# Performance work log

Hardware: AMD Instinct MI355X
Metric: run time of the kernel (lower is better)

## Reference

```python
import jax, jax.numpy as jnp
import numpy as np

D_ATOM, D_MODEL, H = 128, 512, 4
D_H = D_ATOM // H
D_FF = 4 * D_ATOM
EPS = 1e-5


def _ln(x, g, b):
    m = jnp.mean(x, axis=-1, keepdims=True)
    v = jnp.mean((x - m) ** 2, axis=-1, keepdims=True)
    return (x - m) / jnp.sqrt(v + EPS) * g + b


def setup_inputs() -> dict:
    key = jax.random.key(0)
    ks = jax.random.split(key, 20)
    B, N_ATOM, N_PAIRS, N_TOK = 2, 2048, 16384, 512
    c_atom = jax.random.normal(ks[0], (B, N_ATOM, D_ATOM), dtype=jnp.float32)
    p_lm = jax.random.normal(ks[1], (B, N_PAIRS, 16), dtype=jnp.float32)
    p_lm_idx = jax.random.randint(ks[2], (B, N_PAIRS, 2), 0, N_ATOM, dtype=jnp.int32)
    token_idx = jnp.sort(jax.random.randint(ks[3], (B, N_ATOM), 0, N_TOK, dtype=jnp.int32), axis=-1)
    s = 0.05
    w = lambda k, sh: jax.random.normal(k, sh, dtype=jnp.float32) * s
    return {
        'c_atom': c_atom, 'p_lm': p_lm, 'p_lm_idx': p_lm_idx,
        'token_idx': token_idx, 'n_tokens': N_TOK,
        'ln_attn_g': jnp.ones((D_ATOM,), jnp.float32), 'ln_attn_b': jnp.zeros((D_ATOM,), jnp.float32),
        'w_q': w(ks[4], (D_ATOM, D_ATOM)), 'w_k': w(ks[5], (D_ATOM, D_ATOM)),
        'w_v': w(ks[6], (D_ATOM, D_ATOM)), 'w_g': w(ks[7], (D_ATOM, D_ATOM)),
        'w_o': w(ks[8], (D_ATOM, D_ATOM)),
        'pb_w': w(ks[9], (16, H)), 'pb_b': jnp.zeros((H,), jnp.float32),
        'ln_ff_g': jnp.ones((D_ATOM,), jnp.float32), 'ln_ff_b': jnp.zeros((D_ATOM,), jnp.float32),
        'sw_w1': w(ks[10], (D_ATOM, D_FF)), 'sw_w2': w(ks[11], (D_ATOM, D_FF)),
        'sw_w3': w(ks[12], (D_FF, D_ATOM)),
        'tok_w': w(ks[13], (D_ATOM, D_MODEL)), 'tok_b': jnp.zeros((D_MODEL,), jnp.float32),
    }


def reference(c_atom, p_lm, p_lm_idx, token_idx, n_tokens,
              ln_attn_g, ln_attn_b, w_q, w_k, w_v, w_g, w_o, pb_w, pb_b,
              ln_ff_g, ln_ff_b, sw_w1, sw_w2, sw_w3, tok_w, tok_b):
    B, N, _ = c_atom.shape
    q_n = _ln(c_atom, ln_attn_g, ln_attn_b)
    Q = (q_n @ w_q).reshape(B, N, H, D_H)
    K = (q_n @ w_k).reshape(B, N, H, D_H)
    V = (q_n @ w_v).reshape(B, N, H, D_H)
    G = q_n @ w_g  # (B, N, d_atom)

    scores = jnp.einsum('bihd,bjhd->bhij', Q, K) / jnp.sqrt(jnp.float32(D_H))

    bias = p_lm @ pb_w + pb_b  # (B, P, H)
    def scat(src, dst, b_):
        return jnp.zeros((H, N, N), b_.dtype).at[:, src, dst].set(b_.T)
    pair_bias = jax.vmap(scat)(p_lm_idx[..., 0], p_lm_idx[..., 1], bias)
    scores = scores + pair_bias

    token_mask = token_idx[:, :, None] == token_idx[:, None, :]  # (B,N,N)
    scores = jnp.where(token_mask[:, None], scores, -jnp.inf)
    attn = jax.nn.softmax(scores, axis=-1)
    attn = jnp.nan_to_num(attn)

    att_out = jnp.einsum('bhij,bjhd->bihd', attn, V).reshape(B, N, D_ATOM)
    q = c_atom + jax.nn.sigmoid(G) * (att_out @ w_o)
    h = _ln(q, ln_ff_g, ln_ff_b)
    q = q + (jax.nn.silu(h @ sw_w1) * (h @ sw_w2)) @ sw_w3
    atom_feat = q @ tok_w + tok_b  # (B, N, d_model)

    seg = (token_idx + jnp.arange(B, dtype=token_idx.dtype)[:, None] * n_tokens).reshape(-1)
    sums = jax.ops.segment_sum(atom_feat.reshape(B * N, D_MODEL), seg, num_segments=B * n_tokens)
    cnts = jax.ops.segment_sum(jnp.ones((B * N,), atom_feat.dtype), seg, num_segments=B * n_tokens)
    out = sums / jnp.maximum(cnts, 1.0)[:, None]
    return out.reshape(B, n_tokens, D_MODEL)
```

## Files before the change

kernel.cpp:

```cpp
#include <hip/hip_runtime.h>
#include <hip/hip_bf16.h>
#include <math.h>

#define B_     2
#define N_     2048
#define DA     128
#define H_     4
#define DH     32
#define DFF    512
#define DM     512
#define NT     512
#define NP     16384
#define MAXL   32
#define LDSP   136
#define PVS    40

typedef short bf16x8 __attribute__((ext_vector_type(8)));
typedef float f32x4  __attribute__((ext_vector_type(4)));

__device__ __forceinline__ short bf16r(float x) {
    union { float f; unsigned u; } v; v.f = x;
    unsigned r = v.u + 0x7FFFu + ((v.u >> 16) & 1u);
    return (short)(r >> 16);
}
__device__ __forceinline__ float bf2f(short h) {
    union { unsigned u; float f; } v;
    v.u = ((unsigned)(unsigned short)h) << 16;
    return v.f;
}

__global__ __launch_bounds__(1024) void setup_kernel(
        const float* __restrict__ wq, const float* __restrict__ wk,
        const float* __restrict__ wv, const float* __restrict__ wg,
        const float* __restrict__ wo, const float* __restrict__ w1,
        const float* __restrict__ w2, const float* __restrict__ w3,
        const float* __restrict__ tw, const int* __restrict__ tok,
        const int* __restrict__ pidx,
        const float* __restrict__ c_atom, const float* __restrict__ lng,
        const float* __restrict__ lnb,
        short* __restrict__ pqkvg, short* __restrict__ pwo,
        short* __restrict__ pw12, short* __restrict__ pw3,
        short* __restrict__ ptok, short* __restrict__ hln,
        int* __restrict__ cnt, int* __restrict__ tst,
        int* __restrict__ win) {
    __shared__ int c[1024];
    __shared__ int sb[1024];
    if (blockIdx.x < 42) {
        int gid = blockIdx.x * 1024 + threadIdx.x;
        int lane = gid & 63;
        int grp = gid >> 6;
        int quad = lane >> 4, nn = lane & 15;
        const float* src; short* dst; int stride;
        if (grp < 128) {
            int g = grp; int kt = g & 3, nt = g >> 2;
            int n = nt * 16 + nn;
            const float* w = (n < 128) ? wq : (n < 256) ? wk : (n < 384) ? wv : wg;
            src = w + (kt * 32 + quad * 8) * 128 + (n & 127);
            dst = pqkvg + (g * 64 + lane) * 8;
            stride = 128;
        } else if (grp < 160) {
            int g = grp - 128; int kt = g & 3, nt = g >> 2;
            src = wo + (kt * 32 + quad * 8) * 128 + nt * 16 + nn;
            dst = pwo + (g * 64 + lane) * 8;
            stride = 128;
        } else if (grp < 416) {
            int g = grp - 160; int kt = g & 3, nt = g >> 2;
            int n = nt * 16 + nn;
            src = ((n & 1) ? w2 : w1) + (kt * 32 + quad * 8) * 512 + (n >> 1);
            dst = pw12 + (g * 64 + lane) * 8;
            stride = 512;
        } else if (grp < 544) {
            int g = grp - 416; int kt = g & 15, nt = g >> 4;
            src = w3 + (kt * 32 + quad * 8) * 128 + nt * 16 + nn;
            dst = pw3 + (g * 64 + lane) * 8;
            stride = 128;
        } else {
            int g = grp - 544; int kt = g & 3, nt = g >> 2;
            src = tw + (kt * 32 + quad * 8) * 512 + nt * 16 + nn;
            dst = ptok + (g * 64 + lane) * 8;
            stride = 512;
        }
#pragma unroll
        for (int j = 0; j < 8; j++) dst[j] = bf16r(src[j * stride]);
    } else if (blockIdx.x == 42) {
        int tid = threadIdx.x;
        c[tid] = 0;
        __syncthreads();
#pragma unroll
        for (int i = 0; i < 4; i++) {
            int idx = tid + i * 1024;
            int b = idx >> 11;
            atomicAdd(&c[b * NT + tok[idx]], 1);
        }
        __syncthreads();
        int t = tid & (NT - 1);
        int v = c[tid];
        int* cur = c;
        int* alt = sb;
        for (int d = 1; d < NT; d <<= 1) {
            int y = cur[tid];
            if (t >= d) y += cur[tid - d];
            alt[tid] = y;
            __syncthreads();
            int* tmp = cur; cur = alt; alt = tmp;
        }
        tst[tid] = cur[tid] - v;
        cnt[tid] = v;
    } else if (blockIdx.x < 75) {
        int p = (blockIdx.x - 43) * 1024 + threadIdx.x;
        int b = p >> 14, pp = p & (NP - 1);
        int src = pidx[p * 2], dst = pidx[p * 2 + 1];
        if (tok[b * N_ + src] == tok[b * N_ + dst])
            atomicMax(&win[(b * N_ + src) * MAXL + (dst & 31)], pp + 1);
    } else {
        int t = threadIdx.x;
        int rowg = (blockIdx.x - 75) * 256 + (t >> 2);
        int sub = t & 3;
        const float* xr = c_atom + rowg * DA + sub * 32;
        float4 v[8];
        float s = 0.f, sq = 0.f;
#pragma unroll
        for (int i = 0; i < 8; i++) {
            v[i] = *(const float4*)(xr + i * 4);
            s  += v[i].x + v[i].y + v[i].z + v[i].w;
            sq += v[i].x * v[i].x + v[i].y * v[i].y + v[i].z * v[i].z + v[i].w * v[i].w;
        }
        s += __shfl_xor(s, 1); sq += __shfl_xor(sq, 1);
        s += __shfl_xor(s, 2); sq += __shfl_xor(sq, 2);
        float mean = s * (1.f / 128.f);
        float var = sq * (1.f / 128.f) - mean * mean;
        float inv = rsqrtf(var + 1e-5f);
        const float* gp = lng + sub * 32;
        const float* bp = lnb + sub * 32;
        short* dst = hln + rowg * DA + sub * 32;
#pragma unroll
        for (int i = 0; i < 8; i++) {
            dst[i * 4 + 0] = bf16r((v[i].x - mean) * inv * gp[i * 4 + 0] + bp[i * 4 + 0]);
            dst[i * 4 + 1] = bf16r((v[i].y - mean) * inv * gp[i * 4 + 1] + bp[i * 4 + 1]);
            dst[i * 4 + 2] = bf16r((v[i].z - mean) * inv * gp[i * 4 + 2] + bp[i * 4 + 2]);
            dst[i * 4 + 3] = bf16r((v[i].w - mean) * inv * gp[i * 4 + 3] + bp[i * 4 + 3]);
        }
    }
}

__global__ __launch_bounds__(1024) void biasfill(
        const int* __restrict__ pidx, const int* __restrict__ tok,
        const int* __restrict__ win, const float* __restrict__ plm,
        const float* __restrict__ pbw, const float* __restrict__ pbb,
        float* __restrict__ biasT) {
    int p = blockIdx.x * 1024 + threadIdx.x;
    int b = p >> 14, pp = p & (NP - 1);
    int src = pidx[p * 2], dst = pidx[p * 2 + 1];
    if (tok[b * N_ + src] != tok[b * N_ + dst]) return;
    int key = (b * N_ + src) * MAXL + (dst & 31);
    if (win[key] != pp + 1) return;
    const float* pl = plm + (size_t)p * 16;
#pragma unroll
    for (int h = 0; h < H_; h++) {
        float bs = pbb[h];
#pragma unroll
        for (int f = 0; f < 16; f++) bs += pl[f] * pbw[f * H_ + h];
        biasT[(size_t)key * 4 + h] = bs;
    }
}

template<int KT, int KTB, int NTT, int STR>
__device__ __forceinline__ void gemm_a(const short* __restrict__ Abase,
                                       const short* __restrict__ Bp,
                                       int nt0, int lane, f32x4* acc) {
    const short* arow = Abase + (lane & 15) * STR + (lane >> 4) * 8;
    const short* bbase = Bp + lane * 8;
#pragma unroll
    for (int kt = 0; kt < KT; kt++) {
        bf16x8 a = *(const bf16x8*)(arow + kt * 32);
#pragma unroll
        for (int nt = 0; nt < NTT; nt++) {
            bf16x8 b = *(const bf16x8*)(bbase + ((nt0 + nt) * KTB + kt) * 512);
            acc[nt] = __builtin_amdgcn_mfma_f32_16x16x32_bf16(a, b, acc[nt], 0, 0, 0);
        }
    }
}

__global__ __launch_bounds__(256, 2) void tokfused(
        const short* __restrict__ hln, const float* __restrict__ c_atom,
        const float* __restrict__ biasT,
        const int* __restrict__ tst, const int* __restrict__ cnt,
        const int* __restrict__ win,
        const short* __restrict__ pqkvg, const short* __restrict__ pwo,
        const short* __restrict__ pw12, const short* __restrict__ pw3,
        const short* __restrict__ ptok,
        const float* __restrict__ lnfg, const float* __restrict__ lnfb,
        const float* __restrict__ tb, float* __restrict__ out) {
    __shared__ __align__(16) char arena[54272];
    short* As  = (short*)(arena + 0);
    short* Qs  = (short*)(arena + 8704);
    short* Ps  = (short*)(arena + 8704);
    short* Ks  = (short*)(arena + 18944);
    short* VT  = (short*)(arena + 27648);
    float* sgf = (float*)(arena + 37888);
    float* valf = (float*)(arena + 8704);
    short* us   = (short*)(arena + 27648);
    short* q2s  = (short*)(arena + 0);
    short* mrs  = (short*)(arena + 25088);

    int token = blockIdx.x;
    int b = token >> 9;
    int tid = threadIdx.x;
    int lane = tid & 63, wave = tid >> 6;
    int quad = lane >> 4, cc = lane & 15;
    int start = tst[token];
    int L = cnt[token]; if (L > MAXL) L = MAXL;
    const bool fast = (L <= 16);

    {
        int row = tid >> 3, sub = tid & 7;
        int4 v0 = {0,0,0,0}, v1 = {0,0,0,0};
        if (row < L) {
            const int4* src = (const int4*)(hln + (size_t)(b * N_ + start + row) * DA + sub * 16);
            v0 = src[0]; v1 = src[1];
        }
        int4* dst = (int4*)(As + row * LDSP + sub * 16);
        dst[0] = v0; dst[1] = v1;
        if (fast) {
            int4* vz = (int4*)(arena + 27648);
            int4 zz = {0,0,0,0};
#pragma unroll
            for (int k = 0; k < 3; k++) {
                int idx = tid + k * 256;
                if (idx < 640) vz[idx] = zz;
            }
        }
    }
    __syncthreads();

    {
        f32x4 a0[8], a1[8];
#pragma unroll
        for (int i = 0; i < 8; i++)
#pragma unroll
            for (int r = 0; r < 4; r++) { a0[i][r] = 0.f; a1[i][r] = 0.f; }
        gemm_a<4, 4, 8, LDSP>(As, pqkvg, wave * 8, lane, a0);
        if (!fast) gemm_a<4, 4, 8, LDSP>(As + 16 * LDSP, pqkvg, wave * 8, lane, a1);
#pragma unroll
        for (int rt = 0; rt < 2; rt++) {
            if (rt == 1 && fast) break;
            f32x4* ac = rt ? a1 : a0;
#pragma unroll
            for (int nt = 0; nt < 8; nt++) {
                int lc = nt * 16 + cc;
#pragma unroll
                for (int r = 0; r < 4; r++) {
                    int lrow = rt * 16 + quad * 4 + r;
                    float v = ac[nt][r];
                    if (wave == 3)      sgf[lrow * 128 + lc] = 1.f / (1.f + __expf(-v));
                    else if (wave == 0) Qs[lrow * LDSP + lc] = bf16r(v);
                    else if (wave == 1) Ks[lrow * LDSP + lc] = bf16r(v);
                    else VT[(lc >> 5) * 32 * PVS + (lc & 31) * PVS + lrow] = bf16r(v);
                }
            }
        }
    }
    __syncthreads();

    {
        int h = wave;
        const float scale = 0.17677669529663687f;
        int rb = lane & 15;
        f32x4 z = {0.f, 0.f, 0.f, 0.f};
        bf16x8 qa0 = *(const bf16x8*)(Qs + rb * LDSP + h * 32 + quad * 8);
        bf16x8 kb0 = *(const bf16x8*)(Ks + rb * LDSP + h * 32 + quad * 8);
        f32x4 sc00 = __builtin_amdgcn_mfma_f32_16x16x32_bf16(qa0, kb0, z, 0, 0, 0);
        f32x4 sc01 = z, sc10 = z, sc11 = z;
        if (!fast) {
            bf16x8 qa1 = *(const bf16x8*)(Qs + (16 + rb) * LDSP + h * 32 + quad * 8);
            bf16x8 kb1 = *(const bf16x8*)(Ks + (16 + rb) * LDSP + h * 32 + quad * 8);
            sc01 = __builtin_amdgcn_mfma_f32_16x16x32_bf16(qa0, kb1, z, 0, 0, 0);
            sc10 = __builtin_amdgcn_mfma_f32_16x16x32_bf16(qa1, kb0, z, 0, 0, 0);
            sc11 = __builtin_amdgcn_mfma_f32_16x16x32_bf16(qa1, kb1, z, 0, 0, 0);
        }
        __syncthreads();
        short* Ph = Ps + h * 32 * PVS;
        int j0 = cc, j1 = 16 + cc;
#pragma unroll
        for (int it = 0; it < 2; it++) {
            if (it == 1 && fast) break;
            f32x4 sj0 = it ? sc10 : sc00;
            f32x4 sj1 = it ? sc11 : sc01;
#pragma unroll
            for (int r = 0; r < 4; r++) {
                int i = it * 16 + quad * 4 + r;
                int at = start + i; if (at > N_ - 1) at = N_ - 1;
                const int* wrow = win + (size_t)(b * N_ + at) * MAXL;
                const float* brow = biasT + (size_t)(b * N_ + at) * MAXL * 4;
                float s0 = sj0[r] * scale;
                float s1 = fast ? -1e30f : sj1[r] * scale;
                int pw0 = (j0 < L) ? wrow[(start + j0) & 31] : 0;
                if (pw0 > 0) s0 += brow[((start + j0) & 31) * 4 + h];
                if (!fast) {
                    int pw1 = (j1 < L) ? wrow[(start + j1) & 31] : 0;
                    if (pw1 > 0) s1 += brow[((start + j1) & 31) * 4 + h];
                    if (j1 >= L) s1 = -1e30f;
                }
                if (j0 >= L) s0 = -1e30f;
                float m = fmaxf(s0, s1);
                m = fmaxf(m, __shfl_xor(m, 1));
                m = fmaxf(m, __shfl_xor(m, 2));
                m = fmaxf(m, __shfl_xor(m, 4));
                m = fmaxf(m, __shfl_xor(m, 8));
                float e0 = __expf(s0 - m), e1 = __expf(s1 - m);
                float sm = e0 + e1;
                sm += __shfl_xor(sm, 1);
                sm += __shfl_xor(sm, 2);
                sm += __shfl_xor(sm, 4);
                sm += __shfl_xor(sm, 8);
                float inv = 1.f / sm;
                Ph[i * PVS + j0] = bf16r(e0 * inv);
                Ph[i * PVS + j1] = bf16r(e1 * inv);
            }
        }
        __syncthreads();
        const short* Vh = VT + h * 32 * PVS;
        bf16x8 va0 = *(const bf16x8*)(Vh + rb * PVS + quad * 8);
        bf16x8 va1 = *(const bf16x8*)(Vh + (16 + rb) * PVS + quad * 8);
        bf16x8 pb0 = *(const bf16x8*)(Ph + rb * PVS + quad * 8);
        f32x4 ot00 = __builtin_amdgcn_mfma_f32_16x16x32_bf16(va0, pb0, z, 0, 0, 0);
        f32x4 ot10 = __builtin_amdgcn_mfma_f32_16x16x32_bf16(va1, pb0, z, 0, 0, 0);
#pragma unroll
        for (int r = 0; r < 4; r++) {
            As[cc * LDSP + h * 32 + quad * 4 + r]      = bf16r(ot00[r]);
            As[cc * LDSP + h * 32 + 16 + quad * 4 + r] = bf16r(ot10[r]);
        }
        if (!fast) {
            bf16x8 pb1 = *(const bf16x8*)(Ph + (16 + rb) * PVS + quad * 8);
            f32x4 ot01 = __builtin_amdgcn_mfma_f32_16x16x32_bf16(va0, pb1, z, 0, 0, 0);
            f32x4 ot11 = __builtin_amdgcn_mfma_f32_16x16x32_bf16(va1, pb1, z, 0, 0, 0);
#pragma unroll
            for (int r = 0; r < 4; r++) {
                As[(16 + cc) * LDSP + h * 32 + quad * 4 + r]      = bf16r(ot01[r]);
                As[(16 + cc) * LDSP + h * 32 + 16 + quad * 4 + r] = bf16r(ot11[r]);
            }
        }
    }
    __syncthreads();

    if (!fast || wave < 2) {
        f32x4 a3[4];
#pragma unroll
        for (int i = 0; i < 4; i++)
#pragma unroll
            for (int r = 0; r < 4; r++) a3[i][r] = 0.f;
        gemm_a<4, 4, 4, LDSP>(As + (wave >> 1) * 16 * LDSP, pwo, (wave & 1) * 4, lane, a3);
#pragma unroll
        for (int ntl = 0; ntl < 4; ntl++) {
            int gcol = ((wave & 1) * 4 + ntl) * 16 + cc;
#pragma unroll
            for (int r = 0; r < 4; r++) {
                int lrow = (wave >> 1) * 16 + quad * 4 + r;
                int garow = start + lrow; if (garow > N_ - 1) garow = N_ - 1;
                float v = c_atom[(size_t)(b * N_ + garow) * DA + gcol]
                        + sgf[lrow * 128 + gcol] * a3[ntl][r];
                valf[lrow * 128 + gcol] = v;
            }
        }
    }
    __syncthreads();

    {
        int row = tid >> 3, sub = tid & 7;
        if (!fast || row < 16) {
            const float* vr = valf + row * 128 + sub * 16;
            float4 x[4];
            float s = 0.f, sq = 0.f;
#pragma unroll
            for (int i = 0; i < 4; i++) {
                x[i] = *(const float4*)(vr + i * 4);
                s  += x[i].x + x[i].y + x[i].z + x[i].w;
                sq += x[i].x * x[i].x + x[i].y * x[i].y + x[i].z * x[i].z + x[i].w * x[i].w;
            }
            s += __shfl_xor(s, 1); sq += __shfl_xor(sq, 1);
            s += __shfl_xor(s, 2); sq += __shfl_xor(sq, 2);
            s += __shfl_xor(s, 4); sq += __shfl_xor(sq, 4);
            float mean = s * (1.f / 128.f);
            float var = sq * (1.f / 128.f) - mean * mean;
            float inv = rsqrtf(var + 1e-5f);
            short* hr = As + row * LDSP + sub * 16;
            const float* gp = lnfg + sub * 16;
            const float* bp = lnfb + sub * 16;
#pragma unroll
            for (int i = 0; i < 4; i++) {
                hr[i * 4 + 0] = bf16r((x[i].x - mean) * inv * gp[i * 4 + 0] + bp[i * 4 + 0]);
                hr[i * 4 + 1] = bf16r((x[i].y - mean) * inv * gp[i * 4 + 1] + bp[i * 4 + 1]);
                hr[i * 4 + 2] = bf16r((x[i].z - mean) * inv * gp[i * 4 + 2] + bp[i * 4 + 2]);
                hr[i * 4 + 3] = bf16r((x[i].w - mean) * inv * gp[i * 4 + 3] + bp[i * 4 + 3]);
            }
        }
    }
    __syncthreads();

    f32x4 c3a[4];
#pragma unroll
    for (int i = 0; i < 4; i++)
#pragma unroll
        for (int r = 0; r < 4; r++) c3a[i][r] = 0.f;
#pragma unroll
    for (int ch = 0; ch < 2; ch++) {
        f32x4 u0[8], u1[8];
#pragma unroll
        for (int i = 0; i < 8; i++)
#pragma unroll
            for (int r = 0; r < 4; r++) { u0[i][r] = 0.f; u1[i][r] = 0.f; }
        const short* bp12 = pw12 + ch * 32 * 4 * 512;
        gemm_a<4, 4, 8, LDSP>(As, bp12, wave * 8, lane, u0);
        if (!fast) gemm_a<4, 4, 8, LDSP>(As + 16 * LDSP, bp12, wave * 8, lane, u1);
#pragma unroll
        for (int rt = 0; rt < 2; rt++) {
            if (rt == 1 && fast) break;
            f32x4* ac = rt ? u1 : u0;
#pragma unroll
            for (int nt = 0; nt < 8; nt++) {
                int col8 = (wave * 8 + nt) * 8 + (cc >> 1);
#pragma unroll
                for (int r = 0; r < 4; r++) {
                    float v = ac[nt][r];
                    float p = __shfl_xor(v, 1);
                    if (!(lane & 1)) {
                        float sil = v / (1.f + __expf(-v));
                        us[(rt * 16 + quad * 4 + r) * 264 + col8] = bf16r(sil * p);
                    }
                }
            }
        }
        __syncthreads();
        if (!fast || wave < 2)
            gemm_a<8, 16, 4, 264>(us + (wave >> 1) * 16 * 264, pw3 + ch * 8 * 512,
                                  (wave & 1) * 4, lane, c3a);
        __syncthreads();
    }

    if (!fast || wave < 2) {
#pragma unroll
        for (int ntl = 0; ntl < 4; ntl++) {
            int gcol = ((wave & 1) * 4 + ntl) * 16 + cc;
#pragma unroll
            for (int r = 0; r < 4; r++) {
                int lrow = (wave >> 1) * 16 + quad * 4 + r;
                q2s[lrow * 128 + gcol] = bf16r(valf[lrow * 128 + gcol] + c3a[ntl][r]);
            }
        }
    }
    __syncthreads();

    if (tid < 128) {
        int col = tid;
        float sum = 0.f;
        for (int i = 0; i < L; i++) sum += bf2f(q2s[i * 128 + col]);
        float inv = (L > 0) ? 1.f / (float)L : 0.f;
        mrs[col] = bf16r(sum * inv);
    }
    __syncthreads();

    {
        f32x4 a8[8];
#pragma unroll
        for (int i = 0; i < 8; i++)
#pragma unroll
            for (int r = 0; r < 4; r++) a8[i][r] = 0.f;
        gemm_a<4, 4, 8, LDSP>(mrs, ptok, wave * 8, lane, a8);
        if (quad == 0) {
#pragma unroll
            for (int nt = 0; nt < 8; nt++) {
                int col = (wave * 8 + nt) * 16 + cc;
                out[(size_t)token * DM + col] = a8[nt][0] + tb[col];
            }
        }
    }
}

extern "C" void kernel_launch(void* const* d_in, const int* in_sizes, int n_in,
                              void* d_out, int out_size, void* d_ws, size_t ws_size,
                              hipStream_t stream) {
    const float* c_atom  = (const float*)d_in[0];
    const float* p_lm    = (const float*)d_in[1];
    const int*   p_idx   = (const int*)d_in[2];
    const int*   tok     = (const int*)d_in[3];
    const float* ln_a_g  = (const float*)d_in[5];
    const float* ln_a_b  = (const float*)d_in[6];
    const float* w_q     = (const float*)d_in[7];
    const float* w_k     = (const float*)d_in[8];
    const float* w_v     = (const float*)d_in[9];
    const float* w_g     = (const float*)d_in[10];
    const float* w_o     = (const float*)d_in[11];
    const float* pb_w    = (const float*)d_in[12];
    const float* pb_b    = (const float*)d_in[13];
    const float* ln_f_g  = (const float*)d_in[14];
    const float* ln_f_b  = (const float*)d_in[15];
    const float* sw_w1   = (const float*)d_in[16];
    const float* sw_w2   = (const float*)d_in[17];
    const float* sw_w3   = (const float*)d_in[18];
    const float* tok_w   = (const float*)d_in[19];
    const float* tok_b   = (const float*)d_in[20];
    float* out = (float*)d_out;

    float* ws = (float*)d_ws;
    int*   cnt   = (int*)ws;
    int*   tst   = cnt + 1024;
    int*   win   = tst + 1024;
    short* pqkvg = (short*)(win + 131072);
    short* pwo   = pqkvg + 65536;
    short* pw12  = pwo + 16384;
    short* pw3   = pw12 + 131072;
    short* ptok  = pw3 + 65536;
    short* hln   = ptok + 65536;
    float* biasT = (float*)(hln + 524288);

    setup_kernel<<<91, 1024, 0, stream>>>(w_q, w_k, w_v, w_g, w_o, sw_w1, sw_w2,
                                          sw_w3, tok_w, tok, p_idx,
                                          c_atom, ln_a_g, ln_a_b,
                                          pqkvg, pwo, pw12, pw3, ptok, hln,
                                          cnt, tst, win);

    biasfill<<<32, 1024, 0, stream>>>(p_idx, tok, win, p_lm, pb_w, pb_b, biasT);

    tokfused<<<dim3(B_ * NT), dim3(256), 0, stream>>>(
        hln, c_atom, biasT, tst, cnt, win,
        pqkvg, pwo, pw12, pw3, ptok,
        ln_f_g, ln_f_b, tok_b, out);
}
```

Measured before the change: 166.0 us.

## Pack multiple tokens per block via bin descriptors with block-diagonal attention masking

Instead of one workgroup per token (1024 blocks, each mostly under-filled since tokens average about 4 atoms), the setup kernel now greedily packs consecutive tokens into bins of up to 32 atoms and writes bin descriptors. The fused kernel processes a whole bin and masks attention by comparing per-row token ids. It then does per-token mean pooling and a 32-row output GEMM. Excess blocks exit early. This removes wasted MFMA work on padded rows and the per-block fixed overhead, at the cost of a serial single-thread binning loop in setup and always running the full 32-row path. Occupancy is also raised to 3 blocks per SIMD with slightly reduced LDS.

```diff
diff --git a/kernel.cpp b/kernel.cpp
--- a/kernel.cpp
+++ b/kernel.cpp
@@ -42,7 +42,8 @@
         short* __restrict__ pw12, short* __restrict__ pw3,
         short* __restrict__ ptok, short* __restrict__ hln,
         int* __restrict__ cnt, int* __restrict__ tst,
-        int* __restrict__ win) {
+        int* __restrict__ win, int* __restrict__ desc,
+        int* __restrict__ nbinsp) {
     __shared__ int c[1024];
     __shared__ int sb[1024];
     if (blockIdx.x < 42) {
@@ -106,6 +107,22 @@
         }
         tst[tid] = cur[tid] - v;
         cnt[tid] = v;
+        __syncthreads();
+        c[tid] = v;
+        __syncthreads();
+        if (tid == 0) {
+            int nb = 0, acc = 0, bs = 0;
+            for (int tt = 0; tt < 1024; tt++) {
+                int ct = c[tt]; if (ct > 32) ct = 32;
+                if (tt > bs && (acc + ct > 32 || (tt - bs) >= 32 || tt == 512)) {
+                    desc[nb++] = bs | ((tt - bs) << 16);
+                    bs = tt; acc = 0;
+                }
+                acc += ct;
+            }
+            desc[nb++] = bs | ((1024 - bs) << 16);
+            nbinsp[0] = nb;
+        }
     } else if (blockIdx.x < 75) {
         int p = (blockIdx.x - 43) * 1024 + threadIdx.x;
         int b = p >> 14, pp = p & (NP - 1);
@@ -181,54 +198,57 @@
     }
 }
 
-__global__ __launch_bounds__(256, 2) void tokfused(
+__global__ __launch_bounds__(256, 3) void tokfused(
         const short* __restrict__ hln, const float* __restrict__ c_atom,
-        const float* __restrict__ biasT,
+        const float* __restrict__ biasT, const int* __restrict__ tok,
         const int* __restrict__ tst, const int* __restrict__ cnt,
-        const int* __restrict__ win,
+        const int* __restrict__ win, const int* __restrict__ desc,
+        const int* __restrict__ nbinsp,
         const short* __restrict__ pqkvg, const short* __restrict__ pwo,
         const short* __restrict__ pw12, const short* __restrict__ pw3,
         const short* __restrict__ ptok,
         const float* __restrict__ lnfg, const float* __restrict__ lnfb,
         const float* __restrict__ tb, float* __restrict__ out) {
-    __shared__ __align__(16) char arena[54272];
+    int blk = blockIdx.x;
+    if (blk >= nbinsp[0]) return;
+    __shared__ __align__(16) char arena[52736];
+    __shared__ int stok[32];
+    __shared__ int tcnt[32];
     short* As  = (short*)(arena + 0);
     short* Qs  = (short*)(arena + 8704);
     short* Ps  = (short*)(arena + 8704);
-    short* Ks  = (short*)(arena + 18944);
-    short* VT  = (short*)(arena + 27648);
-    float* sgf = (float*)(arena + 37888);
+    short* Ks  = (short*)(arena + 17408);
+    short* VT  = (short*)(arena + 26112);
+    float* sgf = (float*)(arena + 36352);
     float* valf = (float*)(arena + 8704);
-    short* us   = (short*)(arena + 27648);
+    short* us   = (short*)(arena + 26112);
     short* q2s  = (short*)(arena + 0);
-    short* mrs  = (short*)(arena + 25088);
-
-    int token = blockIdx.x;
-    int b = token >> 9;
+    short* mrs  = (short*)(arena + 17408);
+
+    int d = desc[blk];
+    int t0 = d & 0xFFFF, ntok = d >> 16;
+    int b = t0 >> 9;
     int tid = threadIdx.x;
     int lane = tid & 63, wave = tid >> 6;
     int quad = lane >> 4, cc = lane & 15;
-    int start = tst[token];
-    int L = cnt[token]; if (L > MAXL) L = MAXL;
-    const bool fast = (L <= 16);
+    int astart = tst[t0];
+    int tlast = t0 + ntok - 1;
+    int R = tst[tlast] + cnt[tlast] - astart;
+    if (R > 32) R = 32;
 
     {
         int row = tid >> 3, sub = tid & 7;
         int4 v0 = {0,0,0,0}, v1 = {0,0,0,0};
-        if (row < L) {
-            const int4* src = (const int4*)(hln + (size_t)(b * N_ + start + row) * DA + sub * 16);
+        if (row < R) {
+            const int4* src = (const int4*)(hln + (size_t)(b * N_ + astart + row) * DA + sub * 16);
             v0 = src[0]; v1 = src[1];
         }
         int4* dst = (int4*)(As + row * LDSP + sub * 16);
         dst[0] = v0; dst[1] = v1;
-        if (fast) {
-            int4* vz = (int4*)(arena + 27648);
-            int4 zz = {0,0,0,0};
-#pragma unroll
-            for (int k = 0; k < 3; k++) {
-                int idx = tid + k * 256;
-                if (idx < 640) vz[idx] = zz;
-            }
+        if (tid < 32) {
+            stok[tid] = (tid < R) ? tok[b * N_ + astart + tid] : (0x40000000 + tid);
+            int n = (tid < ntok) ? cnt[t0 + tid] : 0;
+            tcnt[tid] = (n > 32) ? 32 : n;
         }
     }
     __syncthreads();
@@ -240,10 +260,9 @@
 #pragma unroll
             for (int r = 0; r < 4; r++) { a0[i][r] = 0.f; a1[i][r] = 0.f; }
         gemm_a<4, 4, 8, LDSP>(As, pqkvg, wave * 8, lane, a0);
-        if (!fast) gemm_a<4, 4, 8, LDSP>(As + 16 * LDSP, pqkvg, wave * 8, lane, a1);
+        gemm_a<4, 4, 8, LDSP>(As + 16 * LDSP, pqkvg, wave * 8, lane, a1);
 #pragma unroll
         for (int rt = 0; rt < 2; rt++) {
-            if (rt == 1 && fast) break;
             f32x4* ac = rt ? a1 : a0;
 #pragma unroll
             for (int nt = 0; nt < 8; nt++) {
@@ -268,40 +287,36 @@
         int rb = lane & 15;
         f32x4 z = {0.f, 0.f, 0.f, 0.f};
         bf16x8 qa0 = *(const bf16x8*)(Qs + rb * LDSP + h * 32 + quad * 8);
+        bf16x8 qa1 = *(const bf16x8*)(Qs + (16 + rb) * LDSP + h * 32 + quad * 8);
         bf16x8 kb0 = *(const bf16x8*)(Ks + rb * LDSP + h * 32 + quad * 8);
+        bf16x8 kb1 = *(const bf16x8*)(Ks + (16 + rb) * LDSP + h * 32 + quad * 8);
         f32x4 sc00 = __builtin_amdgcn_mfma_f32_16x16x32_bf16(qa0, kb0, z, 0, 0, 0);
-        f32x4 sc01 = z, sc10 = z, sc11 = z;
-        if (!fast) {
-            bf16x8 qa1 = *(const bf16x8*)(Qs + (16 + rb) * LDSP + h * 32 + quad * 8);
-            bf16x8 kb1 = *(const bf16x8*)(Ks + (16 + rb) * LDSP + h * 32 + quad * 8);
-            sc01 = __builtin_amdgcn_mfma_f32_16x16x32_bf16(qa0, kb1, z, 0, 0, 0);
-            sc10 = __builtin_amdgcn_mfma_f32_16x16x32_bf16(qa1, kb0, z, 0, 0, 0);
-            sc11 = __builtin_amdgcn_mfma_f32_16x16x32_bf16(qa1, kb1, z, 0, 0, 0);
-        }
+        f32x4 sc01 = __builtin_amdgcn_mfma_f32_16x16x32_bf16(qa0, kb1, z, 0, 0, 0);
+        f32x4 sc10 = __builtin_amdgcn_mfma_f32_16x16x32_bf16(qa1, kb0, z, 0, 0, 0);
+        f32x4 sc11 = __builtin_amdgcn_mfma_f32_16x16x32_bf16(qa1, kb1, z, 0, 0, 0);
         __syncthreads();
         short* Ph = Ps + h * 32 * PVS;
         int j0 = cc, j1 = 16 + cc;
+        int tj0 = stok[j0], tj1 = stok[j1];
 #pragma unroll
         for (int it = 0; it < 2; it++) {
-            if (it == 1 && fast) break;
             f32x4 sj0 = it ? sc10 : sc00;
             f32x4 sj1 = it ? sc11 : sc01;
 #pragma unroll
             for (int r = 0; r < 4; r++) {
                 int i = it * 16 + quad * 4 + r;
-                int at = start + i; if (at > N_ - 1) at = N_ - 1;
-                const int* wrow = win + (size_t)(b * N_ + at) * MAXL;
-                const float* brow = biasT + (size_t)(b * N_ + at) * MAXL * 4;
-                float s0 = sj0[r] * scale;
-                float s1 = fast ? -1e30f : sj1[r] * scale;
-                int pw0 = (j0 < L) ? wrow[(start + j0) & 31] : 0;
-                if (pw0 > 0) s0 += brow[((start + j0) & 31) * 4 + h];
-                if (!fast) {
-                    int pw1 = (j1 < L) ? wrow[(start + j1) & 31] : 0;
-                    if (pw1 > 0) s1 += brow[((start + j1) & 31) * 4 + h];
-                    if (j1 >= L) s1 = -1e30f;
+                int ti = stok[i];
+                int ai = b * N_ + astart + i;
+                float s0 = (tj0 == ti) ? sj0[r] * scale : -1e30f;
+                float s1 = (tj1 == ti) ? sj1[r] * scale : -1e30f;
+                if (tj0 == ti && i < R && j0 < R) {
+                    int key = ai * MAXL + ((astart + j0) & 31);
+                    if (win[key] > 0) s0 += biasT[(size_t)key * 4 + h];
                 }
-                if (j0 >= L) s0 = -1e30f;
+                if (tj1 == ti && i < R && j1 < R) {
+                    int key = ai * MAXL + ((astart + j1) & 31);
+                    if (win[key] > 0) s1 += biasT[(size_t)key * 4 + h];
+                }
                 float m = fmaxf(s0, s1);
                 m = fmaxf(m, __shfl_xor(m, 1));
                 m = fmaxf(m, __shfl_xor(m, 2));
@@ -323,27 +338,22 @@
         bf16x8 va0 = *(const bf16x8*)(Vh + rb * PVS + quad * 8);
         bf16x8 va1 = *(const bf16x8*)(Vh + (16 + rb) * PVS + quad * 8);
         bf16x8 pb0 = *(const bf16x8*)(Ph + rb * PVS + quad * 8);
+        bf16x8 pb1 = *(const bf16x8*)(Ph + (16 + rb) * PVS + quad * 8);
         f32x4 ot00 = __builtin_amdgcn_mfma_f32_16x16x32_bf16(va0, pb0, z, 0, 0, 0);
+        f32x4 ot01 = __builtin_amdgcn_mfma_f32_16x16x32_bf16(va0, pb1, z, 0, 0, 0);
         f32x4 ot10 = __builtin_amdgcn_mfma_f32_16x16x32_bf16(va1, pb0, z, 0, 0, 0);
+        f32x4 ot11 = __builtin_amdgcn_mfma_f32_16x16x32_bf16(va1, pb1, z, 0, 0, 0);
 #pragma unroll
         for (int r = 0; r < 4; r++) {
-            As[cc * LDSP + h * 32 + quad * 4 + r]      = bf16r(ot00[r]);
-            As[cc * LDSP + h * 32 + 16 + quad * 4 + r] = bf16r(ot10[r]);
-        }
-        if (!fast) {
-            bf16x8 pb1 = *(const bf16x8*)(Ph + (16 + rb) * PVS + quad * 8);
-            f32x4 ot01 = __builtin_amdgcn_mfma_f32_16x16x32_bf16(va0, pb1, z, 0, 0, 0);
-            f32x4 ot11 = __builtin_amdgcn_mfma_f32_16x16x32_bf16(va1, pb1, z, 0, 0, 0);
-#pragma unroll
-            for (int r = 0; r < 4; r++) {
-                As[(16 + cc) * LDSP + h * 32 + quad * 4 + r]      = bf16r(ot01[r]);
-                As[(16 + cc) * LDSP + h * 32 + 16 + quad * 4 + r] = bf16r(ot11[r]);
-            }
-        }
-    }
-    __syncthreads();
-
-    if (!fast || wave < 2) {
+            As[cc * LDSP + h * 32 + quad * 4 + r]             = bf16r(ot00[r]);
+            As[cc * LDSP + h * 32 + 16 + quad * 4 + r]        = bf16r(ot10[r]);
+            As[(16 + cc) * LDSP + h * 32 + quad * 4 + r]      = bf16r(ot01[r]);
+            As[(16 + cc) * LDSP + h * 32 + 16 + quad * 4 + r] = bf16r(ot11[r]);
+        }
+    }
+    __syncthreads();
+
+    {
         f32x4 a3[4];
 #pragma unroll
         for (int i = 0; i < 4; i++)
@@ -356,7 +366,7 @@
 #pragma unroll
             for (int r = 0; r < 4; r++) {
                 int lrow = (wave >> 1) * 16 + quad * 4 + r;
-                int garow = start + lrow; if (garow > N_ - 1) garow = N_ - 1;
+                int garow = astart + lrow; if (garow > N_ - 1) garow = N_ - 1;
                 float v = c_atom[(size_t)(b * N_ + garow) * DA + gcol]
                         + sgf[lrow * 128 + gcol] * a3[ntl][r];
                 valf[lrow * 128 + gcol] = v;
@@ -367,32 +377,30 @@
 
     {
         int row = tid >> 3, sub = tid & 7;
-        if (!fast || row < 16) {
-            const float* vr = valf + row * 128 + sub * 16;
-            float4 x[4];
-            float s = 0.f, sq = 0.f;
-#pragma unroll
-            for (int i = 0; i < 4; i++) {
-                x[i] = *(const float4*)(vr + i * 4);
-                s  += x[i].x + x[i].y + x[i].z + x[i].w;
-                sq += x[i].x * x[i].x + x[i].y * x[i].y + x[i].z * x[i].z + x[i].w * x[i].w;
-            }
-            s += __shfl_xor(s, 1); sq += __shfl_xor(sq, 1);
-            s += __shfl_xor(s, 2); sq += __shfl_xor(sq, 2);
-            s += __shfl_xor(s, 4); sq += __shfl_xor(sq, 4);
-            float mean = s * (1.f / 128.f);
-            float var = sq * (1.f / 128.f) - mean * mean;
-            float inv = rsqrtf(var + 1e-5f);
-            short* hr = As + row * LDSP + sub * 16;
-            const float* gp = lnfg + sub * 16;
-            const float* bp = lnfb + sub * 16;
-#pragma unroll
-            for (int i = 0; i < 4; i++) {
-                hr[i * 4 + 0] = bf16r((x[i].x - mean) * inv * gp[i * 4 + 0] + bp[i * 4 + 0]);
-                hr[i * 4 + 1] = bf16r((x[i].y - mean) * inv * gp[i * 4 + 1] + bp[i * 4 + 1]);
-                hr[i * 4 + 2] = bf16r((x[i].z - mean) * inv * gp[i * 4 + 2] + bp[i * 4 + 2]);
-                hr[i * 4 + 3] = bf16r((x[i].w - mean) * inv * gp[i * 4 + 3] + bp[i * 4 + 3]);
-            }
+        const float* vr = valf + row * 128 + sub * 16;
+        float4 x[4];
+        float s = 0.f, sq = 0.f;
+#pragma unroll
+        for (int i = 0; i < 4; i++) {
+            x[i] = *(const float4*)(vr + i * 4);
+            s  += x[i].x + x[i].y + x[i].z + x[i].w;
+            sq += x[i].x * x[i].x + x[i].y * x[i].y + x[i].z * x[i].z + x[i].w * x[i].w;
+        }
+        s += __shfl_xor(s, 1); sq += __shfl_xor(sq, 1);
+        s += __shfl_xor(s, 2); sq += __shfl_xor(sq, 2);
+        s += __shfl_xor(s, 4); sq += __shfl_xor(sq, 4);
+        float mean = s * (1.f / 128.f);
+        float var = sq * (1.f / 128.f) - mean * mean;
+        float inv = rsqrtf(var + 1e-5f);
+        short* hr = As + row * LDSP + sub * 16;
+        const float* gp = lnfg + sub * 16;
+        const float* bp = lnfb + sub * 16;
+#pragma unroll
+        for (int i = 0; i < 4; i++) {
+            hr[i * 4 + 0] = bf16r((x[i].x - mean) * inv * gp[i * 4 + 0] + bp[i * 4 + 0]);
+            hr[i * 4 + 1] = bf16r((x[i].y - mean) * inv * gp[i * 4 + 1] + bp[i * 4 + 1]);
+            hr[i * 4 + 2] = bf16r((x[i].z - mean) * inv * gp[i * 4 + 2] + bp[i * 4 + 2]);
+            hr[i * 4 + 3] = bf16r((x[i].w - mean) * inv * gp[i * 4 + 3] + bp[i * 4 + 3]);
         }
     }
     __syncthreads();
@@ -411,10 +419,9 @@
             for (int r = 0; r < 4; r++) { u0[i][r] = 0.f; u1[i][r] = 0.f; }
         const short* bp12 = pw12 + ch * 32 * 4 * 512;
         gemm_a<4, 4, 8, LDSP>(As, bp12, wave * 8, lane, u0);
-        if (!fast) gemm_a<4, 4, 8, LDSP>(As + 16 * LDSP, bp12, wave * 8, lane, u1);
+        gemm_a<4, 4, 8, LDSP>(As + 16 * LDSP, bp12, wave * 8, lane, u1);
 #pragma unroll
         for (int rt = 0; rt < 2; rt++) {
-            if (rt == 1 && fast) break;
             f32x4* ac = rt ? u1 : u0;
 #pragma unroll
             for (int nt = 0; nt < 8; nt++) {
@@ -431,13 +438,12 @@
             }
         }
         __syncthreads();
-        if (!fast || wave < 2)
-            gemm_a<8, 16, 4, 264>(us + (wave >> 1) * 16 * 264, pw3 + ch * 8 * 512,
-                                  (wave & 1) * 4, lane, c3a);
-        __syncthreads();
-    }
-
-    if (!fast || wave < 2) {
+        gemm_a<8, 16, 4, 264>(us + (wave >> 1) * 16 * 264, pw3 + ch * 8 * 512,
+                              (wave & 1) * 4, lane, c3a);
+        __syncthreads();
+    }
+
+    {
 #pragma unroll
         for (int ntl = 0; ntl < 4; ntl++) {
             int gcol = ((wave & 1) * 4 + ntl) * 16 + cc;
@@ -452,25 +458,37 @@
 
     if (tid < 128) {
         int col = tid;
-        float sum = 0.f;
-        for (int i = 0; i < L; i++) sum += bf2f(q2s[i * 128 + col]);
-        float inv = (L > 0) ? 1.f / (float)L : 0.f;
-        mrs[col] = bf16r(sum * inv);
-    }
-    __syncthreads();
-
-    {
-        f32x4 a8[8];
+        int off = 0;
+        for (int k = 0; k < ntok; k++) {
+            int n = tcnt[k];
+            float sum = 0.f;
+            for (int r2 = 0; r2 < n; r2++) sum += bf2f(q2s[(off + r2) * 128 + col]);
+            off += n;
+            mrs[k * LDSP + col] = bf16r((n > 0) ? sum / (float)n : 0.f);
+        }
+    }
+    __syncthreads();
+
+    {
+        f32x4 a8[8], a8b[8];
 #pragma unroll
         for (int i = 0; i < 8; i++)
 #pragma unroll
-            for (int r = 0; r < 4; r++) a8[i][r] = 0.f;
+            for (int r = 0; r < 4; r++) { a8[i][r] = 0.f; a8b[i][r] = 0.f; }
         gemm_a<4, 4, 8, LDSP>(mrs, ptok, wave * 8, lane, a8);
-        if (quad == 0) {
-#pragma unroll
-            for (int nt = 0; nt < 8; nt++) {
-                int col = (wave * 8 + nt) * 16 + cc;
-                out[(size_t)token * DM + col] = a8[nt][0] + tb[col];
+        if (ntok > 16)
+            gemm_a<4, 4, 8, LDSP>(mrs + 16 * LDSP, ptok, wave * 8, lane, a8b);
+#pragma unroll
+        for (int nt = 0; nt < 8; nt++) {
+            int col = (wave * 8 + nt) * 16 + cc;
+            float bv = tb[col];
+#pragma unroll
+            for (int r = 0; r < 4; r++) {
+                int k = quad * 4 + r;
+                if (k < ntok) out[(size_t)(t0 + k) * DM + col] = a8[nt][r] + bv;
+                int k2 = 16 + quad * 4 + r;
+                if (ntok > 16 && k2 < ntok)
+                    out[(size_t)(t0 + k2) * DM + col] = a8b[nt][r] + bv;
             }
         }
     }
@@ -512,17 +530,19 @@
     short* ptok  = pw3 + 65536;
     short* hln   = ptok + 65536;
     float* biasT = (float*)(hln + 524288);
+    int*   desc  = (int*)(biasT + 524288);
+    int*   nbins = desc + 1025;
 
     setup_kernel<<<91, 1024, 0, stream>>>(w_q, w_k, w_v, w_g, w_o, sw_w1, sw_w2,
                                           sw_w3, tok_w, tok, p_idx,
                                           c_atom, ln_a_g, ln_a_b,
                                           pqkvg, pwo, pw12, pw3, ptok, hln,
-                                          cnt, tst, win);
+                                          cnt, tst, win, desc, nbins);
 
     biasfill<<<32, 1024, 0, stream>>>(p_idx, tok, win, p_lm, pb_w, pb_b, biasT);
 
-    tokfused<<<dim3(B_ * NT), dim3(256), 0, stream>>>(
-        hln, c_atom, biasT, tst, cnt, win,
+    tokfused<<<dim3(1024), dim3(256), 0, stream>>>(
+        hln, c_atom, biasT, tok, tst, cnt, win, desc, nbins,
         pqkvg, pwo, pw12, pw3, ptok,
         ln_f_g, ln_f_b, tok_b, out);
 }
```

New measurement: 247.2 us. 48.9% more time.
